# Kernel optimization log

Measured on AMD Instinct MI355X. Metric: run time of the kernel, lower is better.

## Reference

```python
import jax, jax.numpy as jnp
import numpy as np

H = 512          # hidden_size
B = 1024         # batch
T = 256          # warmup sequence length
NUM_STEPS = 64


def setup_inputs() -> dict:
    key = jax.random.key(0)
    ks = jax.random.split(key, 8)
    bound = 1.0 / np.sqrt(H)  # torch default init for RNN/Linear
    x = jax.random.normal(ks[0], (B, T), dtype=jnp.float32)
    W_ih = jax.random.uniform(ks[1], (H, 1), jnp.float32, -bound, bound)
    W_hh = jax.random.uniform(ks[2], (H, H), jnp.float32, -bound, bound)
    b_ih = jax.random.uniform(ks[3], (H,), jnp.float32, -bound, bound)
    b_hh = jax.random.uniform(ks[4], (H,), jnp.float32, -bound, bound)
    W_fc = jax.random.uniform(ks[5], (1, H), jnp.float32, -bound, bound)
    b_fc = jax.random.uniform(ks[6], (1,), jnp.float32, -bound, bound)
    return {"x": x, "W_ih": W_ih, "W_hh": W_hh, "b_ih": b_ih,
            "b_hh": b_hh, "W_fc": W_fc, "b_fc": b_fc, "num_steps": NUM_STEPS}


def reference(x, W_ih, W_hh, b_ih, b_hh, W_fc, b_fc, num_steps):
    # Phase 1: warmup RNN over the input series. h_t = relu(x_t*W_ih + b_ih + h@W_hh^T + b_hh)
    bias = b_ih + b_hh  # [H]
    w_in = W_ih[:, 0]   # [H], input_size == 1

    def warm_step(h, xt):                      # h: [B,H], xt: [B]
        h = jax.nn.relu(xt[:, None] * w_in[None, :] + h @ W_hh.T + bias)
        return h, None

    h0 = jnp.zeros((B, H), dtype=x.dtype)
    h, _ = jax.lax.scan(warm_step, h0, x.T)    # scan over time: x.T is [T,B]

    def roll_step(h, _):
        y = h @ W_fc.T + b_fc                  # [B,1]
        h = jax.nn.relu(y @ W_ih.T + h @ W_hh.T + bias)
        return h, y

    _, ys = jax.lax.scan(roll_step, h, None, length=num_steps)  # ys: [S,B,1]
    return jnp.transpose(ys, (1, 0, 2))        # [B, num_steps, 1]
```

## Files before the change

### kernel.cpp

```cpp
#include <hip/hip_runtime.h>
#include <stdint.h>

#define H 512
#define B_SZ 1024
#define T_WARM 256
#define NSTEPS 64
#define TOTAL_T (T_WARM + NSTEPS)

#define RPB 16
#define HC 128
#define NTEAM 64
#define NCG 4
#define NBLK 256
#define NTHR 512
#define HSTR 520

typedef __attribute__((ext_vector_type(8))) short bf16x8;
typedef __attribute__((ext_vector_type(4))) float f32x4;

__device__ __forceinline__ ushort f2bf(float f) {
    uint32_t u = __builtin_bit_cast(uint32_t, f);
    u += 0x7FFFu + ((u >> 16) & 1u);
    return (ushort)(u >> 16);
}
__device__ __forceinline__ float bf2f(ushort h) {
    uint32_t u = ((uint32_t)h) << 16;
    return __builtin_bit_cast(float, u);
}

__global__ void prep_kernel(const float* __restrict__ x,
                            const float* __restrict__ W_hh,
                            const float* __restrict__ b_ih,
                            const float* __restrict__ b_hh,
                            ushort* __restrict__ Wh, ushort* __restrict__ Wl,
                            float* __restrict__ bias, float* __restrict__ xT,
                            uint32_t* __restrict__ Hb0, uint32_t* __restrict__ flags) {
    int i = blockIdx.x * NTHR + threadIdx.x;
    Hb0[i] = 0u;
    if (i < 4096) flags[i] = 0u;
    if (i < H * H) {
        float w = W_hh[i];
        ushort hi = f2bf(w);
        float rem = w - bf2f(hi);
        Wh[i] = hi;
        Wl[i] = f2bf(rem);
    }
    if (i < B_SZ * T_WARM) {
        int b = i & (B_SZ - 1), t = i >> 10;
        xT[t * B_SZ + b] = x[b * T_WARM + t];
    }
    if (i < H) bias[i] = b_ih[i] + b_hh[i];
}

__global__ __launch_bounds__(NTHR, 1)
void rnn_kernel(const float* __restrict__ xT,
                const float* __restrict__ W_ih,
                const float* __restrict__ b_fc_p,
                const float* __restrict__ W_fc,
                const ushort* __restrict__ Wh_g,
                const ushort* __restrict__ Wl_g,
                const float* __restrict__ bias_g,
                uint32_t* __restrict__ Hb0, uint32_t* __restrict__ Hb1,
                uint32_t* __restrict__ flags,
                float* __restrict__ out) {
    __shared__ ushort h_hi[2][RPB * HSTR];
    __shared__ ushort h_lo[2][RPB * HSTR];
    __shared__ uint32_t tr[RPB * HC];
    __shared__ float w_fc_s[H];
    __shared__ float w_in_s[HC];
    __shared__ float bias_s[HC];
    __shared__ float sx[RPB];
    __shared__ float sy[RPB];

    const int tid = threadIdx.x;
    const int bid = blockIdx.x;
    const int team = bid & (NTEAM - 1);
    const int cg = bid >> 6;
    const int row0 = team * RPB;
    const int col0 = cg * HC;

    w_fc_s[tid & (H - 1)] = W_fc[tid & (H - 1)];
    if (tid < HC) { w_in_s[tid] = W_ih[col0 + tid]; bias_s[tid] = bias_g[col0 + tid]; }
    const float bfc = b_fc_p[0];

    const int lane = tid & 63;
    const int wv = tid >> 6;
    const int n = lane & 15, q = lane >> 4;

    bf16x8 Bh[16], Bl[16];
    {
        const ushort* wh = Wh_g + (col0 + wv * 16 + n) * H + q * 8;
        const ushort* wl = Wl_g + (col0 + wv * 16 + n) * H + q * 8;
        #pragma unroll
        for (int kt = 0; kt < 16; ++kt) {
            Bh[kt] = *(const bf16x8*)(wh + kt * 32);
            Bl[kt] = *(const bf16x8*)(wl + kt * 32);
        }
    }

    uint32_t* myflag = flags + (team * NCG + cg) * 16;
    const uint32_t* pollflag = flags + (team * NCG + (wv >> 1)) * 16;
    const bool selfw = ((wv >> 1) == cg);

    for (int t = 0; t < TOTAL_T; ++t) {
        float xv = 0.f;
        if (t < T_WARM && tid < RPB) xv = xT[t * B_SZ + row0 + tid];

        uint64_t tmp[8];
        if (t > 0 && selfw) {
            #pragma unroll
            for (int it = 0; it < 8; ++it) {
                int idx = it * 64 + lane;
                int r = idx >> 5, cpair = idx & 31;
                int kloc = (wv & 1) * 64 + cpair * 2;
                const uint32_t* p = &tr[r * HC + kloc];
                tmp[it] = (uint64_t)p[0] | ((uint64_t)p[1] << 32);
            }
        } else {
            if (t > 0) {
                while (__hip_atomic_load(pollflag, __ATOMIC_RELAXED, __HIP_MEMORY_SCOPE_AGENT)
                       < (uint32_t)t)
                    __builtin_amdgcn_s_sleep(1);
            }
            const uint32_t* hb = (t & 1) ? Hb1 : Hb0;
            const uint64_t* src = (const uint64_t*)hb;
            #pragma unroll
            for (int it = 0; it < 8; ++it) {
                int idx = it * 64 + lane;
                int r = idx >> 5, cpair = idx & 31;
                tmp[it] = __hip_atomic_load(src + ((row0 + r) * 256 + wv * 32 + cpair),
                                            __ATOMIC_RELAXED, __HIP_MEMORY_SCOPE_AGENT);
            }
        }

        ushort* hhb = h_hi[t & 1];
        ushort* hlb = h_lo[t & 1];
        #pragma unroll
        for (int it = 0; it < 8; ++it) {
            int idx = it * 64 + lane;
            int r = idx >> 5, cpair = idx & 31;
            int k = wv * 64 + cpair * 2;
            uint64_t u = tmp[it];
            uint32_t w0 = (uint32_t)u, w1 = (uint32_t)(u >> 32);
            uint32_t hw = (w0 >> 16) | (w1 & 0xFFFF0000u);
            uint32_t lw = (w0 & 0xFFFFu) | (w1 << 16);
            *(uint32_t*)(&hhb[r * HSTR + k]) = hw;
            *(uint32_t*)(&hlb[r * HSTR + k]) = lw;
        }
        if (t < T_WARM && tid < RPB) sx[tid] = xv;
        __syncthreads();

        if (t >= T_WARM) {
            if (tid < RPB * 16) {
                int r = tid >> 4, seg = tid & 15;
                const ushort* hh = &hhb[r * HSTR];
                const ushort* hl = &hlb[r * HSTR];
                float s = 0.f;
                #pragma unroll
                for (int kk = 0; kk < 32; ++kk) {
                    int k = seg + kk * 16;
                    s += (bf2f(hh[k]) + bf2f(hl[k])) * w_fc_s[k];
                }
                #pragma unroll
                for (int off = 8; off; off >>= 1) s += __shfl_down(s, off, 16);
                if (seg == 0) {
                    float y = s + bfc;
                    sy[r] = y;
                    if (cg == 0) out[(row0 + r) * NSTEPS + (t - T_WARM)] = y;
                }
            }
            __syncthreads();
        }

        f32x4 acc0 = {0.f, 0.f, 0.f, 0.f}, acc1 = {0.f, 0.f, 0.f, 0.f};
        const ushort* ha = &hhb[n * HSTR] + q * 8;
        const ushort* la = &hlb[n * HSTR] + q * 8;
        #pragma unroll
        for (int kt = 0; kt < 16; kt += 2) {
            {
                bf16x8 ah = *(const bf16x8*)(ha + kt * 32);
                bf16x8 al = *(const bf16x8*)(la + kt * 32);
                acc0 = __builtin_amdgcn_mfma_f32_16x16x32_bf16(ah, Bh[kt], acc0, 0, 0, 0);
                acc0 = __builtin_amdgcn_mfma_f32_16x16x32_bf16(al, Bh[kt], acc0, 0, 0, 0);
                acc0 = __builtin_amdgcn_mfma_f32_16x16x32_bf16(ah, Bl[kt], acc0, 0, 0, 0);
            }
            {
                bf16x8 ah = *(const bf16x8*)(ha + (kt + 1) * 32);
                bf16x8 al = *(const bf16x8*)(la + (kt + 1) * 32);
                acc1 = __builtin_amdgcn_mfma_f32_16x16x32_bf16(ah, Bh[kt + 1], acc1, 0, 0, 0);
                acc1 = __builtin_amdgcn_mfma_f32_16x16x32_bf16(al, Bh[kt + 1], acc1, 0, 0, 0);
                acc1 = __builtin_amdgcn_mfma_f32_16x16x32_bf16(ah, Bl[kt + 1], acc1, 0, 0, 0);
            }
        }

        const int jl = wv * 16 + n;
        const float wi = w_in_s[jl], bj = bias_s[jl];
        uint32_t* dst = ((t & 1) ? Hb0 : Hb1) + col0 + jl;
        #pragma unroll
        for (int i = 0; i < 4; ++i) {
            int m = q * 4 + i;
            float sv = (t < T_WARM) ? sx[m] : sy[m];
            float v = acc0[i] + acc1[i] + sv * wi + bj;
            v = fmaxf(v, 0.f);
            ushort hi = f2bf(v);
            float rem = v - bf2f(hi);
            uint32_t u = ((uint32_t)hi << 16) | (uint32_t)f2bf(rem);
            tr[m * HC + jl] = u;
            __hip_atomic_store(dst + (row0 + m) * H, u, __ATOMIC_RELAXED, __HIP_MEMORY_SCOPE_AGENT);
        }
        __syncthreads();
        if (tid == 0)
            __hip_atomic_store(myflag, (uint32_t)(t + 1), __ATOMIC_RELAXED, __HIP_MEMORY_SCOPE_AGENT);
    }
}

extern "C" void kernel_launch(void* const* d_in, const int* in_sizes, int n_in,
                              void* d_out, int out_size, void* d_ws, size_t ws_size,
                              hipStream_t stream) {
    const float* x    = (const float*)d_in[0];
    const float* W_ih = (const float*)d_in[1];
    const float* W_hh = (const float*)d_in[2];
    const float* b_ih = (const float*)d_in[3];
    const float* b_hh = (const float*)d_in[4];
    const float* W_fc = (const float*)d_in[5];
    const float* b_fc = (const float*)d_in[6];
    float* out = (float*)d_out;

    uint8_t* w = (uint8_t*)d_ws;
    ushort*   Wh    = (ushort*)(w);
    ushort*   Wl    = (ushort*)(w + 524288);
    float*    bias  = (float*)(w + 1048576);
    float*    xT    = (float*)(w + 1052672);
    uint32_t* Hb0   = (uint32_t*)(w + 2101248);
    uint32_t* Hb1   = (uint32_t*)(w + 4198400);
    uint32_t* flags = (uint32_t*)(w + 6295552);

    prep_kernel<<<1024, NTHR, 0, stream>>>(x, W_hh, b_ih, b_hh, Wh, Wl, bias, xT, Hb0, flags);
    rnn_kernel<<<NBLK, NTHR, 0, stream>>>(xT, W_ih, b_fc, W_fc, Wh, Wl, bias, Hb0, Hb1, flags, out);
}
```

Baseline: 1.000 ms.

## Split global hidden-state exchange into separate hi/lo bf16 planes with wide stores

The global hidden-state exchange buffers change from interleaved 32-bit hi|lo words to separate hi and lo bf16 planes. Producers first stage results in LDS, then repack them and write 64-bit atomic stores per thread, adding one extra barrier. Consumers load contiguous 64-bit chunks straight into the LDS hi/lo tiles without unpacking. The aim is fewer, wider global atomic ops and less per-step shuffling on the latency-critical cross-block exchange, at the cost of an additional __syncthreads per step.

```diff
diff --git a/kernel.cpp b/kernel.cpp
--- a/kernel.cpp
+++ b/kernel.cpp
@@ -34,9 +34,10 @@
                             const float* __restrict__ b_hh,
                             ushort* __restrict__ Wh, ushort* __restrict__ Wl,
                             float* __restrict__ bias, float* __restrict__ xT,
-                            uint32_t* __restrict__ Hb0, uint32_t* __restrict__ flags) {
+                            uint32_t* __restrict__ Hhi0, uint32_t* __restrict__ Hlo0,
+                            uint32_t* __restrict__ flags) {
     int i = blockIdx.x * NTHR + threadIdx.x;
-    Hb0[i] = 0u;
+    if (i < B_SZ * 256) { Hhi0[i] = 0u; Hlo0[i] = 0u; }
     if (i < 4096) flags[i] = 0u;
     if (i < H * H) {
         float w = W_hh[i];
@@ -60,7 +61,8 @@
                 const ushort* __restrict__ Wh_g,
                 const ushort* __restrict__ Wl_g,
                 const float* __restrict__ bias_g,
-                uint32_t* __restrict__ Hb0, uint32_t* __restrict__ Hb1,
+                uint32_t* __restrict__ Hhi0, uint32_t* __restrict__ Hhi1,
+                uint32_t* __restrict__ Hlo0, uint32_t* __restrict__ Hlo1,
                 uint32_t* __restrict__ flags,
                 float* __restrict__ out) {
     __shared__ ushort h_hi[2][RPB * HSTR];
@@ -102,19 +104,29 @@
     const uint32_t* pollflag = flags + (team * NCG + (wv >> 1)) * 16;
     const bool selfw = ((wv >> 1) == cg);
 
+    const int sr = lane & 15;
+    const int sg = lane >> 4;
+
     for (int t = 0; t < TOTAL_T; ++t) {
         float xv = 0.f;
         if (t < T_WARM && tid < RPB) xv = xT[t * B_SZ + row0 + tid];
 
-        uint64_t tmp[8];
+        ushort* hhb = h_hi[t & 1];
+        ushort* hlb = h_lo[t & 1];
+
         if (t > 0 && selfw) {
             #pragma unroll
             for (int it = 0; it < 8; ++it) {
                 int idx = it * 64 + lane;
                 int r = idx >> 5, cpair = idx & 31;
                 int kloc = (wv & 1) * 64 + cpair * 2;
-                const uint32_t* p = &tr[r * HC + kloc];
-                tmp[it] = (uint64_t)p[0] | ((uint64_t)p[1] << 32);
+                uint32_t w0 = tr[r * HC + kloc];
+                uint32_t w1 = tr[r * HC + kloc + 1];
+                uint32_t hw = (w0 >> 16) | (w1 & 0xFFFF0000u);
+                uint32_t lw = (w0 & 0xFFFFu) | (w1 << 16);
+                int k = wv * 64 + cpair * 2;
+                *(uint32_t*)(&hhb[r * HSTR + k]) = hw;
+                *(uint32_t*)(&hlb[r * HSTR + k]) = lw;
             }
         } else {
             if (t > 0) {
@@ -122,30 +134,22 @@
                        < (uint32_t)t)
                     __builtin_amdgcn_s_sleep(1);
             }
-            const uint32_t* hb = (t & 1) ? Hb1 : Hb0;
-            const uint64_t* src = (const uint64_t*)hb;
-            #pragma unroll
-            for (int it = 0; it < 8; ++it) {
-                int idx = it * 64 + lane;
-                int r = idx >> 5, cpair = idx & 31;
-                tmp[it] = __hip_atomic_load(src + ((row0 + r) * 256 + wv * 32 + cpair),
-                                            __ATOMIC_RELAXED, __HIP_MEMORY_SCOPE_AGENT);
-            }
-        }
-
-        ushort* hhb = h_hi[t & 1];
-        ushort* hlb = h_lo[t & 1];
-        #pragma unroll
-        for (int it = 0; it < 8; ++it) {
-            int idx = it * 64 + lane;
-            int r = idx >> 5, cpair = idx & 31;
-            int k = wv * 64 + cpair * 2;
-            uint64_t u = tmp[it];
-            uint32_t w0 = (uint32_t)u, w1 = (uint32_t)(u >> 32);
-            uint32_t hw = (w0 >> 16) | (w1 & 0xFFFF0000u);
-            uint32_t lw = (w0 & 0xFFFFu) | (w1 << 16);
-            *(uint32_t*)(&hhb[r * HSTR + k]) = hw;
-            *(uint32_t*)(&hlb[r * HSTR + k]) = lw;
+            const uint64_t* srch = (const uint64_t*)((t & 1) ? Hhi1 : Hhi0);
+            const uint64_t* srcl = (const uint64_t*)((t & 1) ? Hlo1 : Hlo0);
+            const int bu = (row0 + sr) * 128 + wv * 16 + sg * 4;
+            uint64_t th[4], tl[4];
+            #pragma unroll
+            for (int j = 0; j < 4; ++j)
+                th[j] = __hip_atomic_load(srch + bu + j, __ATOMIC_RELAXED, __HIP_MEMORY_SCOPE_AGENT);
+            #pragma unroll
+            for (int j = 0; j < 4; ++j)
+                tl[j] = __hip_atomic_load(srcl + bu + j, __ATOMIC_RELAXED, __HIP_MEMORY_SCOPE_AGENT);
+            #pragma unroll
+            for (int j = 0; j < 4; ++j) {
+                int k = wv * 64 + sg * 16 + j * 4;
+                *(uint64_t*)(&hhb[sr * HSTR + k]) = th[j];
+                *(uint64_t*)(&hlb[sr * HSTR + k]) = tl[j];
+            }
         }
         if (t < T_WARM && tid < RPB) sx[tid] = xv;
         __syncthreads();
@@ -195,7 +199,6 @@
 
         const int jl = wv * 16 + n;
         const float wi = w_in_s[jl], bj = bias_s[jl];
-        uint32_t* dst = ((t & 1) ? Hb0 : Hb1) + col0 + jl;
         #pragma unroll
         for (int i = 0; i < 4; ++i) {
             int m = q * 4 + i;
@@ -204,9 +207,23 @@
             v = fmaxf(v, 0.f);
             ushort hi = f2bf(v);
             float rem = v - bf2f(hi);
-            uint32_t u = ((uint32_t)hi << 16) | (uint32_t)f2bf(rem);
-            tr[m * HC + jl] = u;
-            __hip_atomic_store(dst + (row0 + m) * H, u, __ATOMIC_RELAXED, __HIP_MEMORY_SCOPE_AGENT);
+            tr[m * HC + jl] = ((uint32_t)hi << 16) | (uint32_t)f2bf(rem);
+        }
+        __syncthreads();
+
+        {
+            int r = tid >> 5, seg = tid & 31;
+            const uint32_t* tp = &tr[r * HC + seg * 4];
+            uint32_t w0 = tp[0], w1 = tp[1], w2 = tp[2], w3 = tp[3];
+            uint64_t hu = (uint64_t)((w0 >> 16) | (w1 & 0xFFFF0000u))
+                        | ((uint64_t)((w2 >> 16) | (w3 & 0xFFFF0000u)) << 32);
+            uint64_t lu = (uint64_t)((w0 & 0xFFFFu) | (w1 << 16))
+                        | ((uint64_t)((w2 & 0xFFFFu) | (w3 << 16)) << 32);
+            uint64_t* dsth = (uint64_t*)((t & 1) ? Hhi0 : Hhi1);
+            uint64_t* dstl = (uint64_t*)((t & 1) ? Hlo0 : Hlo1);
+            int du = (row0 + r) * 128 + cg * 32 + seg;
+            __hip_atomic_store(dsth + du, hu, __ATOMIC_RELAXED, __HIP_MEMORY_SCOPE_AGENT);
+            __hip_atomic_store(dstl + du, lu, __ATOMIC_RELAXED, __HIP_MEMORY_SCOPE_AGENT);
         }
         __syncthreads();
         if (tid == 0)
@@ -231,10 +248,13 @@
     ushort*   Wl    = (ushort*)(w + 524288);
     float*    bias  = (float*)(w + 1048576);
     float*    xT    = (float*)(w + 1052672);
-    uint32_t* Hb0   = (uint32_t*)(w + 2101248);
-    uint32_t* Hb1   = (uint32_t*)(w + 4198400);
+    uint32_t* Hhi0  = (uint32_t*)(w + 2101248);
+    uint32_t* Hhi1  = (uint32_t*)(w + 3149824);
+    uint32_t* Hlo0  = (uint32_t*)(w + 4198400);
+    uint32_t* Hlo1  = (uint32_t*)(w + 5246976);
     uint32_t* flags = (uint32_t*)(w + 6295552);
 
-    prep_kernel<<<1024, NTHR, 0, stream>>>(x, W_hh, b_ih, b_hh, Wh, Wl, bias, xT, Hb0, flags);
-    rnn_kernel<<<NBLK, NTHR, 0, stream>>>(xT, W_ih, b_fc, W_fc, Wh, Wl, bias, Hb0, Hb1, flags, out);
-}
+    prep_kernel<<<1024, NTHR, 0, stream>>>(x, W_hh, b_ih, b_hh, Wh, Wl, bias, xT, Hhi0, Hlo0, flags);
+    rnn_kernel<<<NBLK, NTHR, 0, stream>>>(xT, W_ih, b_fc, W_fc, Wh, Wl, bias,
+                                          Hhi0, Hhi1, Hlo0, Hlo1, flags, out);
+}
```

Result: slower. 1.304 ms (+30.4%).

## Split hidden dim across 8 column groups with packed flag polling

Applied to the files above, without the earlier changes.

Doubles the number of column groups per team (HC 128→64, 512 blocks of 256 threads, two blocks per CU), so each block owns fewer output columns and the MFMA work spreads across more CUs. The per-team flags are packed contiguously so each wave polls two producers with one 64-bit load. Each wave now reads a full 128-column slice per row from global memory. The LDS self-forwarding path via `tr` is removed, so a block's own columns now also come back through global memory. This trades more inter-block synchronization traffic and global reads for more parallelism per timestep.

```diff
diff --git a/kernel.cpp b/kernel.cpp
--- a/kernel.cpp
+++ b/kernel.cpp
@@ -8,11 +8,11 @@
 #define TOTAL_T (T_WARM + NSTEPS)
 
 #define RPB 16
-#define HC 128
+#define HC 64
 #define NTEAM 64
-#define NCG 4
-#define NBLK 256
-#define NTHR 512
+#define NCG 8
+#define NBLK 512
+#define NTHR 256
 #define HSTR 520
 
 typedef __attribute__((ext_vector_type(8))) short bf16x8;
@@ -35,7 +35,7 @@
                             ushort* __restrict__ Wh, ushort* __restrict__ Wl,
                             float* __restrict__ bias, float* __restrict__ xT,
                             uint32_t* __restrict__ Hb0, uint32_t* __restrict__ flags) {
-    int i = blockIdx.x * NTHR + threadIdx.x;
+    int i = blockIdx.x * 512 + threadIdx.x;
     Hb0[i] = 0u;
     if (i < 4096) flags[i] = 0u;
     if (i < H * H) {
@@ -52,7 +52,7 @@
     if (i < H) bias[i] = b_ih[i] + b_hh[i];
 }
 
-__global__ __launch_bounds__(NTHR, 1)
+__global__ __launch_bounds__(NTHR, 2)
 void rnn_kernel(const float* __restrict__ xT,
                 const float* __restrict__ W_ih,
                 const float* __restrict__ b_fc_p,
@@ -65,7 +65,6 @@
                 float* __restrict__ out) {
     __shared__ ushort h_hi[2][RPB * HSTR];
     __shared__ ushort h_lo[2][RPB * HSTR];
-    __shared__ uint32_t tr[RPB * HC];
     __shared__ float w_fc_s[H];
     __shared__ float w_in_s[HC];
     __shared__ float bias_s[HC];
@@ -79,7 +78,7 @@
     const int row0 = team * RPB;
     const int col0 = cg * HC;
 
-    w_fc_s[tid & (H - 1)] = W_fc[tid & (H - 1)];
+    for (int i = tid; i < H; i += NTHR) w_fc_s[i] = W_fc[i];
     if (tid < HC) { w_in_s[tid] = W_ih[col0 + tid]; bias_s[tid] = bias_g[col0 + tid]; }
     const float bfc = b_fc_p[0];
 
@@ -98,52 +97,42 @@
         }
     }
 
-    uint32_t* myflag = flags + (team * NCG + cg) * 16;
-    const uint32_t* pollflag = flags + (team * NCG + (wv >> 1)) * 16;
-    const bool selfw = ((wv >> 1) == cg);
+    uint32_t* myflag = flags + team * 16 + cg;
+    const uint64_t* pollp = (const uint64_t*)(flags + team * 16 + 2 * wv);
+    const bool s0 = (2 * wv == cg), s1 = (2 * wv + 1 == cg);
 
     for (int t = 0; t < TOTAL_T; ++t) {
         float xv = 0.f;
         if (t < T_WARM && tid < RPB) xv = xT[t * B_SZ + row0 + tid];
 
-        uint64_t tmp[8];
-        if (t > 0 && selfw) {
-            #pragma unroll
-            for (int it = 0; it < 8; ++it) {
-                int idx = it * 64 + lane;
-                int r = idx >> 5, cpair = idx & 31;
-                int kloc = (wv & 1) * 64 + cpair * 2;
-                const uint32_t* p = &tr[r * HC + kloc];
-                tmp[it] = (uint64_t)p[0] | ((uint64_t)p[1] << 32);
-            }
-        } else {
-            if (t > 0) {
-                while (__hip_atomic_load(pollflag, __ATOMIC_RELAXED, __HIP_MEMORY_SCOPE_AGENT)
-                       < (uint32_t)t)
-                    __builtin_amdgcn_s_sleep(1);
-            }
+        if (t > 0) {
+            const uint32_t tt = (uint32_t)t;
+            for (;;) {
+                uint64_t f = __hip_atomic_load(pollp, __ATOMIC_RELAXED, __HIP_MEMORY_SCOPE_AGENT);
+                uint32_t f0 = (uint32_t)f, f1 = (uint32_t)(f >> 32);
+                if ((s0 || f0 >= tt) && (s1 || f1 >= tt)) break;
+                __builtin_amdgcn_s_sleep(1);
+            }
+        }
+
+        uint64_t tmp[16];
+        {
             const uint32_t* hb = (t & 1) ? Hb1 : Hb0;
             const uint64_t* src = (const uint64_t*)hb;
             #pragma unroll
-            for (int it = 0; it < 8; ++it) {
-                int idx = it * 64 + lane;
-                int r = idx >> 5, cpair = idx & 31;
-                tmp[it] = __hip_atomic_load(src + ((row0 + r) * 256 + wv * 32 + cpair),
-                                            __ATOMIC_RELAXED, __HIP_MEMORY_SCOPE_AGENT);
-            }
-        }
-
+            for (int r = 0; r < 16; ++r)
+                tmp[r] = __hip_atomic_load(src + (row0 + r) * 256 + wv * 64 + lane,
+                                           __ATOMIC_RELAXED, __HIP_MEMORY_SCOPE_AGENT);
+        }
         ushort* hhb = h_hi[t & 1];
         ushort* hlb = h_lo[t & 1];
         #pragma unroll
-        for (int it = 0; it < 8; ++it) {
-            int idx = it * 64 + lane;
-            int r = idx >> 5, cpair = idx & 31;
-            int k = wv * 64 + cpair * 2;
-            uint64_t u = tmp[it];
+        for (int r = 0; r < 16; ++r) {
+            uint64_t u = tmp[r];
             uint32_t w0 = (uint32_t)u, w1 = (uint32_t)(u >> 32);
             uint32_t hw = (w0 >> 16) | (w1 & 0xFFFF0000u);
             uint32_t lw = (w0 & 0xFFFFu) | (w1 << 16);
+            int k = wv * 128 + lane * 2;
             *(uint32_t*)(&hhb[r * HSTR + k]) = hw;
             *(uint32_t*)(&hlb[r * HSTR + k]) = lw;
         }
@@ -151,7 +140,7 @@
         __syncthreads();
 
         if (t >= T_WARM) {
-            if (tid < RPB * 16) {
+            {
                 int r = tid >> 4, seg = tid & 15;
                 const ushort* hh = &hhb[r * HSTR];
                 const ushort* hl = &hlb[r * HSTR];
@@ -205,7 +194,6 @@
             ushort hi = f2bf(v);
             float rem = v - bf2f(hi);
             uint32_t u = ((uint32_t)hi << 16) | (uint32_t)f2bf(rem);
-            tr[m * HC + jl] = u;
             __hip_atomic_store(dst + (row0 + m) * H, u, __ATOMIC_RELAXED, __HIP_MEMORY_SCOPE_AGENT);
         }
         __syncthreads();
@@ -235,6 +223,6 @@
     uint32_t* Hb1   = (uint32_t*)(w + 4198400);
     uint32_t* flags = (uint32_t*)(w + 6295552);
 
-    prep_kernel<<<1024, NTHR, 0, stream>>>(x, W_hh, b_ih, b_hh, Wh, Wl, bias, xT, Hb0, flags);
+    prep_kernel<<<1024, 512, 0, stream>>>(x, W_hh, b_ih, b_hh, Wh, Wl, bias, xT, Hb0, flags);
     rnn_kernel<<<NBLK, NTHR, 0, stream>>>(xT, W_ih, b_fc, W_fc, Wh, Wl, bias, Hb0, Hb1, flags, out);
 }
```

Measured after the change: 1.172 ms. 1.17x slower.
